# Kernel optimization log

Hardware: AMD Instinct MI355X
Metric: run time of the kernel (lower is better)

Reference implementation:

```python
import jax, jax.numpy as jnp
import numpy as np

U, I, D = 100000, 50000, 64       # users, items, latdim
H, DH = 4, 16                      # att_head, head dim (D = H*DH)
HN = 128                           # hyperNum
L = 2                              # hgnn_layer
HOPS = 2                           # gcn_hops
SLOPE = 0.5                        # leaky
NNZ_UI = 1000000
NNZ_UU = 1000000


def leaky(x):
    return jnp.where(x >= 0, x, SLOPE * x)


def spmm(rows, cols, vals, X, n_out):
    # sparse COO @ dense: out[r] += vals * X[c]
    return jax.ops.segment_sum(vals[:, None] * X[cols], rows, num_segments=n_out)


def lightgcn(uE, iE, ar, ac, av, tr, tc, tv):
    ulats, ilats = [uE], [iE]
    for _ in range(HOPS):
        tu = spmm(ar, ac, av, ilats[-1], U)
        ti = spmm(tr, tc, tv, ulats[-1], I)
        ulats.append(tu)
        ilats.append(ti)
    return sum(ulats[1:]), sum(ilats[1:])


def lightgcn2(uE, ur, uc, uv):
    lats = [uE]
    for _ in range(HOPS):
        lats.append(spmm(ur, uc, uv, lats[-1], U))
    return sum(lats[1:])


def prepare_key(E, K):
    # [N, D] -> [H, N, DH]
    return (E @ K).reshape(-1, H, DH).transpose(1, 0, 2)


def hg_transformer(E0, Key, Hyper, V, pV, W1, W2):
    # Hyper: [HN, D]; Key: [H, N, DH]
    hyp = Hyper.reshape(HN, H, DH).transpose(1, 2, 0)  # [H, DH, HN]
    total = E0
    cur = E0
    for l in range(L):
        value = (cur @ pV).reshape(-1, H, DH).transpose(1, 2, 0)   # [H, DH, N]
        t1 = ((value @ Key) @ hyp).reshape(D, HN)                  # [D, HN]
        t2 = leaky(t1 @ W1[l].T) + t1                              # Linear(HN,HN) no bias
        t3 = leaky(t2 @ W2[l].T) + t2
        pre = (t3.T @ V).reshape(HN, H, DH).transpose(1, 0, 2)     # [H, HN, DH]
        pre = hyp @ pre                                            # [H, DH, DH]
        new = (Key @ pre).transpose(1, 0, 2).reshape(-1, D)        # [N, D]
        total = total + new
        cur = new
    return total, Hyper


def setup_inputs() -> dict:
    key = jax.random.key(0)
    ks = jax.random.split(key, 14)
    s = 0.05
    uEmbeds0 = jax.random.normal(ks[0], (U, D), jnp.float32) * s
    iEmbeds0 = jax.random.normal(ks[1], (I, D), jnp.float32) * s
    Ks = jax.random.normal(ks[2], (3, D, D), jnp.float32) * (1.0 / np.sqrt(D))
    hg_Hyper = jax.random.normal(ks[3], (3, HN, D), jnp.float32) * s
    hg_V = jax.random.normal(ks[4], (3, D, D), jnp.float32) * (1.0 / np.sqrt(D))
    hg_pV = jax.random.normal(ks[5], (3, D, D), jnp.float32) * (1.0 / np.sqrt(D))
    hg_W1 = jax.random.normal(ks[6], (3, L, HN, HN), jnp.float32) * (1.0 / np.sqrt(HN))
    hg_W2 = jax.random.normal(ks[7], (3, L, HN, HN), jnp.float32) * (1.0 / np.sqrt(HN))
    adj_rows = jax.random.randint(ks[8], (NNZ_UI,), 0, U, jnp.int32)
    adj_cols = jax.random.randint(ks[9], (NNZ_UI,), 0, I, jnp.int32)
    adj_vals = jax.random.uniform(ks[10], (NNZ_UI,), jnp.float32)
    uu_rows = jax.random.randint(ks[11], (NNZ_UU,), 0, U, jnp.int32)
    uu_cols = jax.random.randint(ks[12], (NNZ_UU,), 0, U, jnp.int32)
    uu_vals = jax.random.uniform(ks[13], (NNZ_UU,), jnp.float32)
    return dict(uEmbeds0=uEmbeds0, iEmbeds0=iEmbeds0, Ks=Ks, hg_Hyper=hg_Hyper,
                hg_V=hg_V, hg_pV=hg_pV, hg_W1=hg_W1, hg_W2=hg_W2,
                adj_rows=adj_rows, adj_cols=adj_cols, adj_vals=adj_vals,
                tp_rows=adj_cols, tp_cols=adj_rows, tp_vals=adj_vals,
                uu_rows=uu_rows, uu_cols=uu_cols, uu_vals=uu_vals)


def reference(uEmbeds0, iEmbeds0, Ks, hg_Hyper, hg_V, hg_pV, hg_W1, hg_W2,
              adj_vals, tp_vals, uu_vals,
              adj_rows, adj_cols, tp_rows, tp_cols, uu_rows, uu_cols):
    ui_u_gcn, ui_i_gcn = lightgcn(uEmbeds0, iEmbeds0, adj_rows, adj_cols, adj_vals,
                                  tp_rows, tp_cols, tp_vals)
    uu_gcn = lightgcn2(uEmbeds0, uu_rows, uu_cols, uu_vals)
    ui_uEmbed0 = uEmbeds0 + ui_u_gcn
    ui_iEmbed0 = iEmbeds0 + ui_i_gcn
    uu_Embed0 = uEmbeds0 + uu_gcn
    ui_uKey = prepare_key(ui_uEmbed0, Ks[0])
    ui_iKey = prepare_key(ui_iEmbed0, Ks[1])
    uu_Key = prepare_key(uu_Embed0, Ks[2])
    ui_ulat, ui_uHyper = hg_transformer(ui_uEmbed0, ui_uKey, hg_Hyper[0], hg_V[0], hg_pV[0], hg_W1[0], hg_W2[0])
    ui_ilat, ui_iHyper = hg_transformer(ui_iEmbed0, ui_iKey, hg_Hyper[1], hg_V[1], hg_pV[1], hg_W1[1], hg_W2[1])
    uu_lat, uu_Hyper = hg_transformer(uu_Embed0, uu_Key, hg_Hyper[2], hg_V[2], hg_pV[2], hg_W1[2], hg_W2[2])
    return (ui_uEmbed0, ui_iEmbed0, ui_ulat, ui_ilat, ui_uKey, ui_iKey,
            ui_uHyper, ui_iHyper, uu_Embed0, uu_lat, uu_Key, uu_Hyper)
```

## Files before the change

kernel.cpp:

```cpp
#include <hip/hip_runtime.h>

__global__ __launch_bounds__(256) void spmm_k(const int* __restrict__ rows,
                                              const int* __restrict__ cols,
                                              const float* __restrict__ vals,
                                              const float* __restrict__ X,
                                              float* __restrict__ out, int nnz) {
    int gid = blockIdx.x * 256 + threadIdx.x;
    int e = gid >> 6;
    if (e >= nnz) return;
    int d = gid & 63;
    int r = rows[e], c = cols[e];
    float v = vals[e];
    float x = X[(size_t)c * 64 + d];
    atomicAdd(&out[(size_t)r * 64 + d], v * x);
}

__global__ __launch_bounds__(256) void add3_kernel(const float* __restrict__ base,
                                                   const float* __restrict__ a,
                                                   const float* __restrict__ b,
                                                   float* __restrict__ outb, size_t n) {
    size_t i = (size_t)blockIdx.x * 256 + threadIdx.x;
    if (i >= n) return;
    outb[i] = base[i] + a[i] + b[i];
}

__global__ __launch_bounds__(256) void hist_k(const int* __restrict__ rows,
                                              int* __restrict__ cnt, int nnz) {
    int i = blockIdx.x * 256 + threadIdx.x;
    if (i < nnz) atomicAdd(&cnt[rows[i]], 1);
}

__global__ __launch_bounds__(256) void scan_part(const int* __restrict__ cnt,
                                                 int* __restrict__ bsum, int n) {
    __shared__ int sh[256];
    int tid = threadIdx.x;
    int i = blockIdx.x * 256 + tid;
    sh[tid] = (i < n) ? cnt[i] : 0;
    __syncthreads();
    for (int st = 128; st > 0; st >>= 1) {
        if (tid < st) sh[tid] += sh[tid + st];
        __syncthreads();
    }
    if (tid == 0) bsum[blockIdx.x] = sh[0];
}

__global__ __launch_bounds__(1024) void scan_top(int* __restrict__ b, int nb) {
    __shared__ int sh[1024];
    int tid = threadIdx.x;
    int orig = (tid < nb) ? b[tid] : 0;
    sh[tid] = orig;
    __syncthreads();
    for (int st = 1; st < 1024; st <<= 1) {
        int v = (tid >= st) ? sh[tid - st] : 0;
        __syncthreads();
        sh[tid] += v;
        __syncthreads();
    }
    if (tid < nb) b[tid] = sh[tid] - orig;
}

__global__ __launch_bounds__(256) void scan_final(const int* __restrict__ cnt,
                                                  const int* __restrict__ bsum,
                                                  int* __restrict__ rp,
                                                  int* __restrict__ cur, int n, int nnz) {
    __shared__ int sh[256];
    int tid = threadIdx.x;
    int i = blockIdx.x * 256 + tid;
    int orig = (i < n) ? cnt[i] : 0;
    sh[tid] = orig;
    __syncthreads();
    for (int st = 1; st < 256; st <<= 1) {
        int v = (tid >= st) ? sh[tid - st] : 0;
        __syncthreads();
        sh[tid] += v;
        __syncthreads();
    }
    int ex = sh[tid] - orig + bsum[blockIdx.x];
    if (i < n) { rp[i] = ex; cur[i] = ex; }
    if (i == n - 1) rp[n] = nnz;
}

__global__ __launch_bounds__(256) void scatter_k(const int* __restrict__ rows,
                                                 const int* __restrict__ cols,
                                                 const float* __restrict__ vals,
                                                 int* __restrict__ cur,
                                                 int2* __restrict__ edge, int nnz) {
    int i = blockIdx.x * 256 + threadIdx.x;
    if (i >= nnz) return;
    int p = atomicAdd(&cur[rows[i]], 1);
    edge[p] = make_int2(cols[i], __float_as_int(vals[i]));
}

__global__ __launch_bounds__(256) void spmm_csr(const int* __restrict__ rp,
                                                const int2* __restrict__ edge,
                                                const float* __restrict__ X,
                                                const float* __restrict__ a0,
                                                const float* __restrict__ a1,
                                                float* __restrict__ out, int nrows) {
    int gid = blockIdx.x * 256 + threadIdx.x;
    int r = gid >> 6;
    if (r >= nrows) return;
    int d = gid & 63;
    int s = rp[r], e = rp[r + 1];
    float acc = 0.f;
    int i = s;
    for (; i + 4 <= e; i += 4) {
        int2 e0 = edge[i], e1 = edge[i + 1], e2 = edge[i + 2], e3 = edge[i + 3];
        float x0 = X[(size_t)e0.x * 64 + d];
        float x1 = X[(size_t)e1.x * 64 + d];
        float x2 = X[(size_t)e2.x * 64 + d];
        float x3 = X[(size_t)e3.x * 64 + d];
        acc += __int_as_float(e0.y) * x0;
        acc += __int_as_float(e1.y) * x1;
        acc += __int_as_float(e2.y) * x2;
        acc += __int_as_float(e3.y) * x3;
    }
    for (; i < e; ++i) {
        int2 ee = edge[i];
        acc += __int_as_float(ee.y) * X[(size_t)ee.x * 64 + d];
    }
    size_t o = (size_t)r * 64 + d;
    if (a0) acc += a0[o];
    if (a1) acc += a1[o];
    out[o] = acc;
}

__global__ __launch_bounds__(256) void key_gemm(const float* __restrict__ E,
                                                const float* __restrict__ K,
                                                float* __restrict__ Kout, int N) {
    __shared__ float Ksh[4096];
    int tid = threadIdx.x;
    for (int i = tid; i < 4096; i += 256) Ksh[i] = K[i];
    __syncthreads();
    int j = tid & 63, slot = tid >> 6;
    int n = blockIdx.x * 4 + slot;
    if (n >= N) return;
    const float* Er = E + (size_t)n * 64;
    float acc = 0.f;
#pragma unroll
    for (int kk = 0; kk < 64; ++kk) acc += Er[kk] * Ksh[kk * 64 + j];
    int h = j >> 4, dh = j & 15;
    Kout[((size_t)h * N + n) * 16 + dh] = acc;
}

#define ATB_BLOCKS 512
__global__ __launch_bounds__(256) void atb_part(const float* __restrict__ cur,
                                                const float* __restrict__ Key,
                                                float* __restrict__ part, int N, int chunk) {
    int tid = threadIdx.x;
    int k = tid & 63, h = tid >> 6;
    const float* Kh = Key + (size_t)h * N * 16;
    float acc[16];
#pragma unroll
    for (int i = 0; i < 16; ++i) acc[i] = 0.f;
    int s = blockIdx.x * chunk;
    int e = s + chunk;
    if (e > N) e = N;
#pragma unroll 2
    for (int n = s; n < e; ++n) {
        float c = cur[(size_t)n * 64 + k];
        const float4* kr = (const float4*)(Kh + (size_t)n * 16);
        float4 k0 = kr[0], k1 = kr[1], k2 = kr[2], k3 = kr[3];
        acc[0]  += c * k0.x;  acc[1]  += c * k0.y;  acc[2]  += c * k0.z;  acc[3]  += c * k0.w;
        acc[4]  += c * k1.x;  acc[5]  += c * k1.y;  acc[6]  += c * k1.z;  acc[7]  += c * k1.w;
        acc[8]  += c * k2.x;  acc[9]  += c * k2.y;  acc[10] += c * k2.z;  acc[11] += c * k2.w;
        acc[12] += c * k3.x;  acc[13] += c * k3.y;  acc[14] += c * k3.z;  acc[15] += c * k3.w;
    }
    float4* po = (float4*)(part + (size_t)blockIdx.x * 4096 + k * 64 + h * 16);
    po[0] = make_float4(acc[0],  acc[1],  acc[2],  acc[3]);
    po[1] = make_float4(acc[4],  acc[5],  acc[6],  acc[7]);
    po[2] = make_float4(acc[8],  acc[9],  acc[10], acc[11]);
    po[3] = make_float4(acc[12], acc[13], acc[14], acc[15]);
}

__global__ __launch_bounds__(256) void reduce_m(const float* __restrict__ part,
                                                float* __restrict__ M, int nb) {
    int i = blockIdx.x * 256 + threadIdx.x;
    if (i >= 4096) return;
    float s = 0.f;
#pragma unroll 8
    for (int b = 0; b < nb; ++b) s += part[(size_t)b * 4096 + i];
    M[i] = s;
}

#define ATB_ROWS 128
__global__ __launch_bounds__(256) void atb_k(const float* __restrict__ cur,
                                             const float* __restrict__ Key,
                                             float* __restrict__ M, int N) {
    int tid = threadIdx.x;
    int k = tid & 63, h = tid >> 6;
    const float* Kh = Key + (size_t)h * N * 16;
    float acc[16];
#pragma unroll
    for (int i = 0; i < 16; ++i) acc[i] = 0.f;
    int s = blockIdx.x * ATB_ROWS;
    int e = s + ATB_ROWS;
    if (e > N) e = N;
#pragma unroll 2
    for (int n = s; n < e; ++n) {
        float c = cur[(size_t)n * 64 + k];
        const float4* kr = (const float4*)(Kh + (size_t)n * 16);
        float4 k0 = kr[0], k1 = kr[1], k2 = kr[2], k3 = kr[3];
        acc[0]  += c * k0.x;  acc[1]  += c * k0.y;  acc[2]  += c * k0.z;  acc[3]  += c * k0.w;
        acc[4]  += c * k1.x;  acc[5]  += c * k1.y;  acc[6]  += c * k1.z;  acc[7]  += c * k1.w;
        acc[8]  += c * k2.x;  acc[9]  += c * k2.y;  acc[10] += c * k2.z;  acc[11] += c * k2.w;
        acc[12] += c * k3.x;  acc[13] += c * k3.y;  acc[14] += c * k3.z;  acc[15] += c * k3.w;
    }
#pragma unroll
    for (int d2 = 0; d2 < 16; ++d2)
        atomicAdd(&M[k * 64 + h * 16 + d2], acc[d2]);
}

__global__ __launch_bounds__(256) void vk_small(const float* __restrict__ M,
                                                const float* __restrict__ pV,
                                                float* __restrict__ VK) {
    int i = blockIdx.x * 256 + threadIdx.x;
    if (i >= 1024) return;
    int d2 = i & 15, d1 = (i >> 4) & 15, h = i >> 8;
    float s = 0.f;
#pragma unroll
    for (int k = 0; k < 64; ++k)
        s += pV[k * 64 + h * 16 + d1] * M[k * 64 + h * 16 + d2];
    VK[i] = s;
}

__global__ __launch_bounds__(256) void t1_kernel(const float* __restrict__ VK,
                                                 const float* __restrict__ hyp,
                                                 float* __restrict__ t1) {
    int i = blockIdx.x * 256 + threadIdx.x;
    if (i >= 8192) return;
    int m = i & 127, d = i >> 7;
    int h = d >> 4;
    float s = 0.f;
#pragma unroll
    for (int d2 = 0; d2 < 16; ++d2) s += VK[d * 16 + d2] * hyp[(h * 16 + d2) * 128 + m];
    t1[i] = s;
}

__global__ __launch_bounds__(256) void ff_kernel(const float* __restrict__ tin,
                                                 const float* __restrict__ W,
                                                 float* __restrict__ tout) {
    int i = blockIdx.x * 256 + threadIdx.x;
    if (i >= 8192) return;
    int m = i & 127, d = i >> 7;
    const float* tr = tin + d * 128;
    const float* wr = W + m * 128;
    float s = 0.f;
#pragma unroll
    for (int mm = 0; mm < 128; ++mm) s += tr[mm] * wr[mm];
    float v = (s >= 0.f ? s : 0.5f * s) + tin[i];
    tout[i] = v;
}

__global__ __launch_bounds__(256) void pre0_kernel(const float* __restrict__ t3,
                                                   const float* __restrict__ V,
                                                   float* __restrict__ pre0) {
    int i = blockIdx.x * 256 + threadIdx.x;
    if (i >= 8192) return;
    int dd = i & 63, m = i >> 6;
    float s = 0.f;
#pragma unroll
    for (int d = 0; d < 64; ++d) s += t3[d * 128 + m] * V[d * 64 + dd];
    pre0[m * 64 + dd] = s;
}

__global__ __launch_bounds__(256) void pre2_kernel(const float* __restrict__ hyp,
                                                   const float* __restrict__ pre0,
                                                   float* __restrict__ pre2) {
    int i = blockIdx.x * 256 + threadIdx.x;
    if (i >= 1024) return;
    int d2 = i & 15, d1 = (i >> 4) & 15, h = i >> 8;
    float s = 0.f;
#pragma unroll
    for (int m = 0; m < 128; ++m) s += hyp[(h * 16 + d1) * 128 + m] * pre0[m * 64 + h * 16 + d2];
    pre2[i] = s;
}

__global__ __launch_bounds__(256) void expand0_kernel(const float* __restrict__ Key,
                                                      const float* __restrict__ pre2,
                                                      const float* __restrict__ E0,
                                                      float* __restrict__ nxt,
                                                      float* __restrict__ tot, int N) {
    __shared__ float p2[1024];
    int tid = threadIdx.x;
    for (int i = tid; i < 1024; i += 256) p2[i] = pre2[i];
    __syncthreads();
    int j = tid & 63, slot = tid >> 6;
    int n = blockIdx.x * 4 + slot;
    if (n >= N) return;
    int h = j >> 4, d2 = j & 15;
    const float* kr = Key + ((size_t)h * N + n) * 16;
    float s = 0.f;
#pragma unroll
    for (int d1 = 0; d1 < 16; ++d1) s += kr[d1] * p2[(h * 16 + d1) * 16 + d2];
    size_t o = (size_t)n * 64 + j;
    nxt[o] = s;
    tot[o] = E0[o] + s;
}

__global__ __launch_bounds__(256) void expand1_kernel(const float* __restrict__ Key,
                                                      const float* __restrict__ pre2,
                                                      const float* __restrict__ tot,
                                                      float* __restrict__ outb, int N) {
    __shared__ float p2[1024];
    int tid = threadIdx.x;
    for (int i = tid; i < 1024; i += 256) p2[i] = pre2[i];
    __syncthreads();
    int j = tid & 63, slot = tid >> 6;
    int n = blockIdx.x * 4 + slot;
    if (n >= N) return;
    int h = j >> 4, d2 = j & 15;
    const float* kr = Key + ((size_t)h * N + n) * 16;
    float s = 0.f;
#pragma unroll
    for (int d1 = 0; d1 < 16; ++d1) s += kr[d1] * p2[(h * 16 + d1) * 16 + d2];
    size_t o = (size_t)n * 64 + j;
    outb[o] = tot[o] + s;
}

__global__ __launch_bounds__(256) void hyp_kernel(const float* __restrict__ Hyper,
                                                  float* __restrict__ hyp3,
                                                  float* __restrict__ out,
                                                  size_t off0, size_t off1, size_t off2) {
    int i = blockIdx.x * 256 + threadIdx.x;
    if (i >= 3 * 8192) return;
    int k = i / 8192, r = i % 8192;
    float v = Hyper[i];
    size_t off = (k == 0) ? off0 : ((k == 1) ? off1 : off2);
    out[off + r] = v;
    int m = r >> 6, dcol = r & 63;
    hyp3[k * 8192 + dcol * 128 + m] = v;
}

extern "C" void kernel_launch(void* const* d_in, const int* in_sizes, int n_in,
                              void* d_out, int out_size, void* d_ws, size_t ws_size,
                              hipStream_t stream) {
    const float* uE      = (const float*)d_in[0];
    const float* iE      = (const float*)d_in[1];
    const float* Ks      = (const float*)d_in[2];
    const float* Hyper   = (const float*)d_in[3];
    const float* Vt      = (const float*)d_in[4];
    const float* pV      = (const float*)d_in[5];
    const float* W1      = (const float*)d_in[6];
    const float* W2      = (const float*)d_in[7];
    const int* adj_rows  = (const int*)d_in[8];
    const int* adj_cols  = (const int*)d_in[9];
    const float* adj_vals= (const float*)d_in[10];
    const int* tp_rows   = (const int*)d_in[11];
    const int* tp_cols   = (const int*)d_in[12];
    const float* tp_vals = (const float*)d_in[13];
    const int* uu_rows   = (const int*)d_in[14];
    const int* uu_cols   = (const int*)d_in[15];
    const float* uu_vals = (const float*)d_in[16];

    const int U = in_sizes[0] / 64;
    const int I = in_sizes[1] / 64;
    const int nnz_ui = in_sizes[8];
    const int nnz_uu = in_sizes[14];
    const size_t UD = (size_t)U * 64, ID = (size_t)I * 64;

    float* ws = (float*)d_ws;
    float* B1 = ws;
    float* B2 = B1 + UD;
    float* B3 = B2 + ID;
    float* hyp3 = B2;
    float* VKw  = hyp3 + 3 * 8192;
    float* t1w  = VKw + 1024;
    float* t2w  = t1w + 8192;
    float* t3w  = t2w + 8192;
    float* pre0w = t3w + 8192;
    float* pre2w = pre0w + 8192;
    float* Mw   = pre2w + 1024;

    float* csrf   = B3 + UD;
    int2*  edge_a = (int2*)csrf;
    int2*  edge_t = edge_a + nnz_ui;
    int2*  edge_u = edge_t + nnz_ui;
    int*   rp_a   = (int*)(edge_u + nnz_uu);
    int*   cur_a  = rp_a + (U + 1);
    int*   rp_t   = cur_a + U;
    int*   cur_t  = rp_t + (I + 1);
    int*   rp_u   = cur_t + I;
    int*   cur_u  = rp_u + (U + 1);
    int*   bsum_a = cur_u + U;
    int*   bsum_t = bsum_a + 1024;
    int*   bsum_u = bsum_t + 1024;
    float* partw  = (float*)(bsum_u + 1024);
    size_t need_bytes = (size_t)((char*)(partw + (size_t)ATB_BLOCKS * 4096) - (char*)d_ws);
    const bool use_csr = (ws_size >= need_bytes) &&
                         ((U + 255) / 256 <= 1024) && ((I + 255) / 256 <= 1024);

    float* out = (float*)d_out;
    const size_t o_uE0 = 0;
    const size_t o_iE0 = UD;
    const size_t o_ulat = UD + ID;
    const size_t o_ilat = 2 * UD + ID;
    const size_t o_uKey = 2 * UD + 2 * ID;
    const size_t o_iKey = 3 * UD + 2 * ID;
    const size_t o_uHyp = 3 * UD + 3 * ID;
    const size_t o_iHyp = o_uHyp + 8192;
    const size_t o_uuE0 = o_iHyp + 8192;
    const size_t o_uulat = o_uuE0 + UD;
    const size_t o_uuKey = o_uulat + UD;
    const size_t o_uuHyp = o_uuKey + UD;

    const int gEU = (int)(((size_t)U * 64 + 255) / 256);
    const int gEI = (int)(((size_t)I * 64 + 255) / 256);

    if (use_csr) {
        auto build = [&](const int* rows, const int* cols, const float* vals,
                         int nnz, int n, int* rp, int* cur, int* bsum, int2* edge) {
            int nb = (n + 255) / 256;
            hipMemsetAsync(cur, 0, (size_t)n * sizeof(int), stream);
            hist_k<<<(nnz + 255) / 256, 256, 0, stream>>>(rows, cur, nnz);
            scan_part<<<nb, 256, 0, stream>>>(cur, bsum, n);
            scan_top<<<1, 1024, 0, stream>>>(bsum, nb);
            scan_final<<<nb, 256, 0, stream>>>(cur, bsum, rp, cur, n, nnz);
            scatter_k<<<(nnz + 255) / 256, 256, 0, stream>>>(rows, cols, vals, cur, edge, nnz);
        };
        build(adj_rows, adj_cols, adj_vals, nnz_ui, U, rp_a, cur_a, bsum_a, edge_a);
        build(tp_rows,  tp_cols,  tp_vals,  nnz_ui, I, rp_t, cur_t, bsum_t, edge_t);
        build(uu_rows,  uu_cols,  uu_vals,  nnz_uu, U, rp_u, cur_u, bsum_u, edge_u);

        spmm_csr<<<gEI, 256, 0, stream>>>(rp_t, edge_t, uE, nullptr, nullptr, B2, I);
        spmm_csr<<<gEU, 256, 0, stream>>>(rp_a, edge_a, iE, nullptr, nullptr, B1, U);
        spmm_csr<<<gEU, 256, 0, stream>>>(rp_a, edge_a, B2, uE, B1, out + o_uE0, U);
        spmm_csr<<<gEI, 256, 0, stream>>>(rp_t, edge_t, B1, iE, B2, out + o_iE0, I);
        spmm_csr<<<gEU, 256, 0, stream>>>(rp_u, edge_u, uE, nullptr, nullptr, B1, U);
        spmm_csr<<<gEU, 256, 0, stream>>>(rp_u, edge_u, B1, uE, B1, out + o_uuE0, U);
    } else {
        const int g_ui = (int)(((size_t)nnz_ui * 64 + 255) / 256);
        const int g_uu = (int)(((size_t)nnz_uu * 64 + 255) / 256);
        const int gU = (int)((UD + 255) / 256);
        const int gI = (int)((ID + 255) / 256);
        hipMemsetAsync(B1, 0, UD * sizeof(float), stream);
        spmm_k<<<g_ui, 256, 0, stream>>>(adj_rows, adj_cols, adj_vals, iE, B1, nnz_ui);
        hipMemsetAsync(B2, 0, ID * sizeof(float), stream);
        spmm_k<<<g_ui, 256, 0, stream>>>(tp_rows, tp_cols, tp_vals, uE, B2, nnz_ui);
        hipMemsetAsync(B3, 0, UD * sizeof(float), stream);
        spmm_k<<<g_ui, 256, 0, stream>>>(adj_rows, adj_cols, adj_vals, B2, B3, nnz_ui);
        add3_kernel<<<gU, 256, 0, stream>>>(uE, B1, B3, out + o_uE0, UD);
        hipMemsetAsync(B3, 0, ID * sizeof(float), stream);
        spmm_k<<<g_ui, 256, 0, stream>>>(tp_rows, tp_cols, tp_vals, B1, B3, nnz_ui);
        add3_kernel<<<gI, 256, 0, stream>>>(iE, B2, B3, out + o_iE0, ID);
        hipMemsetAsync(B1, 0, UD * sizeof(float), stream);
        spmm_k<<<g_uu, 256, 0, stream>>>(uu_rows, uu_cols, uu_vals, uE, B1, nnz_uu);
        hipMemsetAsync(B3, 0, UD * sizeof(float), stream);
        spmm_k<<<g_uu, 256, 0, stream>>>(uu_rows, uu_cols, uu_vals, B1, B3, nnz_uu);
        add3_kernel<<<gU, 256, 0, stream>>>(uE, B1, B3, out + o_uuE0, UD);
    }

    hyp_kernel<<<(3 * 8192 + 255) / 256, 256, 0, stream>>>(Hyper, hyp3, out, o_uHyp, o_iHyp, o_uuHyp);

    const int    Narr[3] = { U, I, U };
    const size_t oE[3]   = { o_uE0, o_iE0, o_uuE0 };
    const size_t oK[3]   = { o_uKey, o_iKey, o_uuKey };
    const size_t oL[3]   = { o_ulat, o_ilat, o_uulat };

    for (int k = 0; k < 3; ++k) {
        int N = Narr[k];
        const float* E0k = out + oE[k];
        float* Keyk = out + oK[k];
        const float* Ksk = Ks + k * 4096;
        const float* pVk = pV + k * 4096;
        const float* Vk  = Vt + k * 4096;
        const float* hypk = hyp3 + k * 8192;

        key_gemm<<<(N + 3) / 4, 256, 0, stream>>>(E0k, Ksk, Keyk, N);

        for (int l = 0; l < 2; ++l) {
            const float* W1kl = W1 + (size_t)(k * 2 + l) * 16384;
            const float* W2kl = W2 + (size_t)(k * 2 + l) * 16384;

            if (use_csr) {
                int chunk = (N + ATB_BLOCKS - 1) / ATB_BLOCKS;
                atb_part<<<ATB_BLOCKS, 256, 0, stream>>>(
                    (l == 0) ? E0k : B1, Keyk, partw, N, chunk);
                reduce_m<<<16, 256, 0, stream>>>(partw, Mw, ATB_BLOCKS);
            } else {
                hipMemsetAsync(Mw, 0, 4096 * sizeof(float), stream);
                atb_k<<<(N + ATB_ROWS - 1) / ATB_ROWS, 256, 0, stream>>>(
                    (l == 0) ? E0k : B1, Keyk, Mw, N);
            }
            vk_small<<<4, 256, 0, stream>>>(Mw, pVk, VKw);
            t1_kernel<<<32, 256, 0, stream>>>(VKw, hypk, t1w);
            ff_kernel<<<32, 256, 0, stream>>>(t1w, W1kl, t2w);
            ff_kernel<<<32, 256, 0, stream>>>(t2w, W2kl, t3w);
            pre0_kernel<<<32, 256, 0, stream>>>(t3w, Vk, pre0w);
            pre2_kernel<<<4, 256, 0, stream>>>(hypk, pre0w, pre2w);

            if (l == 0) {
                expand0_kernel<<<(N + 3) / 4, 256, 0, stream>>>(Keyk, pre2w, E0k, B1, B3, N);
            } else {
                expand1_kernel<<<(N + 3) / 4, 256, 0, stream>>>(Keyk, pre2w, B3, out + oL[k], N);
            }
        }
    }
}
```

Baseline: 1.889 ms.

## Batch the three graph branches into combined kernels and fuse the small chain

Merges the CSR build (histogram, scan, scatter), the SpMM hops, the key GEMM, the ATB partial reductions and the expand kernels for all three branches into single launches that pick a segment from the block or row index. The per-layer chain of small matmuls (vk, t1, ff, pre0, pre2) collapses into one chain3 kernel. The aim is to cut the many kernel launches and to let the three independent branches fill the GPU together instead of running one after another. The cost is extra workspace for the concurrent branch buffers, plus branch selection inside the kernels, which adds complexity.

```diff
diff --git a/kernel.cpp b/kernel.cpp
--- a/kernel.cpp
+++ b/kernel.cpp
@@ -1,50 +1,46 @@
 #include <hip/hip_runtime.h>
 
-__global__ __launch_bounds__(256) void spmm_k(const int* __restrict__ rows,
-                                              const int* __restrict__ cols,
-                                              const float* __restrict__ vals,
-                                              const float* __restrict__ X,
-                                              float* __restrict__ out, int nnz) {
-    int gid = blockIdx.x * 256 + threadIdx.x;
-    int e = gid >> 6;
-    if (e >= nnz) return;
-    int d = gid & 63;
-    int r = rows[e], c = cols[e];
-    float v = vals[e];
-    float x = X[(size_t)c * 64 + d];
-    atomicAdd(&out[(size_t)r * 64 + d], v * x);
-}
-
-__global__ __launch_bounds__(256) void add3_kernel(const float* __restrict__ base,
-                                                   const float* __restrict__ a,
-                                                   const float* __restrict__ b,
-                                                   float* __restrict__ outb, size_t n) {
-    size_t i = (size_t)blockIdx.x * 256 + threadIdx.x;
-    if (i >= n) return;
-    outb[i] = base[i] + a[i] + b[i];
-}
-
-__global__ __launch_bounds__(256) void hist_k(const int* __restrict__ rows,
-                                              int* __restrict__ cnt, int nnz) {
+#define ATB_B 256
+
+__global__ __launch_bounds__(256) void hist3(const int* __restrict__ rA,
+                                             const int* __restrict__ rT,
+                                             const int* __restrict__ rU,
+                                             int nnzA, int nnzU,
+                                             int* __restrict__ cntAll, int U, int I) {
     int i = blockIdx.x * 256 + threadIdx.x;
-    if (i < nnz) atomicAdd(&cnt[rows[i]], 1);
-}
-
-__global__ __launch_bounds__(256) void scan_part(const int* __restrict__ cnt,
-                                                 int* __restrict__ bsum, int n) {
+    int tot = 2 * nnzA + nnzU;
+    if (i >= tot) return;
+    if (i < nnzA) atomicAdd(&cntAll[rA[i]], 1);
+    else if (i < 2 * nnzA) atomicAdd(&cntAll[U + rT[i - nnzA]], 1);
+    else atomicAdd(&cntAll[U + I + rU[i - 2 * nnzA]], 1);
+}
+
+__global__ __launch_bounds__(256) void scan_part3(const int* __restrict__ cntAll,
+                                                  int* __restrict__ bsumAll,
+                                                  int U, int I, int nbA, int nbT) {
+    int b = blockIdx.x;
+    int k, lb, n, coff, bsoff;
+    if (b < nbA)            { k = 0; lb = b;             n = U; coff = 0;     bsoff = 0; }
+    else if (b < nbA + nbT) { k = 1; lb = b - nbA;       n = I; coff = U;     bsoff = 1024; }
+    else                    { k = 2; lb = b - nbA - nbT; n = U; coff = U + I; bsoff = 2048; }
+    (void)k;
     __shared__ int sh[256];
     int tid = threadIdx.x;
-    int i = blockIdx.x * 256 + tid;
-    sh[tid] = (i < n) ? cnt[i] : 0;
+    int i = lb * 256 + tid;
+    sh[tid] = (i < n) ? cntAll[coff + i] : 0;
     __syncthreads();
     for (int st = 128; st > 0; st >>= 1) {
         if (tid < st) sh[tid] += sh[tid + st];
         __syncthreads();
     }
-    if (tid == 0) bsum[blockIdx.x] = sh[0];
-}
-
-__global__ __launch_bounds__(1024) void scan_top(int* __restrict__ b, int nb) {
+    if (tid == 0) bsumAll[bsoff + lb] = sh[0];
+}
+
+__global__ __launch_bounds__(1024) void scan_top3(int* __restrict__ bsumAll,
+                                                  int nbA, int nbT, int nbU) {
+    int g = blockIdx.x;
+    int nb = (g == 0) ? nbA : (g == 1 ? nbT : nbU);
+    int* b = bsumAll + g * 1024;
     __shared__ int sh[1024];
     int tid = threadIdx.x;
     int orig = (tid < nb) ? b[tid] : 0;
@@ -59,14 +55,20 @@
     if (tid < nb) b[tid] = sh[tid] - orig;
 }
 
-__global__ __launch_bounds__(256) void scan_final(const int* __restrict__ cnt,
-                                                  const int* __restrict__ bsum,
-                                                  int* __restrict__ rp,
-                                                  int* __restrict__ cur, int n, int nnz) {
+__global__ __launch_bounds__(256) void scan_final3(int* __restrict__ curAll,
+                                                   const int* __restrict__ bsumAll,
+                                                   int* __restrict__ rpAll,
+                                                   int U, int I, int nbA, int nbT,
+                                                   int nnzA, int nnzU) {
+    int b = blockIdx.x;
+    int lb, n, coff, bsoff, rpoff, nnz;
+    if (b < nbA)            { lb = b;             n = U; coff = 0;     bsoff = 0;    rpoff = 0;                 nnz = nnzA; }
+    else if (b < nbA + nbT) { lb = b - nbA;       n = I; coff = U;     bsoff = 1024; rpoff = U + 1;             nnz = nnzA; }
+    else                    { lb = b - nbA - nbT; n = U; coff = U + I; bsoff = 2048; rpoff = (U + 1) + (I + 1); nnz = nnzU; }
     __shared__ int sh[256];
     int tid = threadIdx.x;
-    int i = blockIdx.x * 256 + tid;
-    int orig = (i < n) ? cnt[i] : 0;
+    int i = lb * 256 + tid;
+    int orig = (i < n) ? curAll[coff + i] : 0;
     sh[tid] = orig;
     __syncthreads();
     for (int st = 1; st < 256; st <<= 1) {
@@ -75,37 +77,51 @@
         sh[tid] += v;
         __syncthreads();
     }
-    int ex = sh[tid] - orig + bsum[blockIdx.x];
-    if (i < n) { rp[i] = ex; cur[i] = ex; }
-    if (i == n - 1) rp[n] = nnz;
-}
-
-__global__ __launch_bounds__(256) void scatter_k(const int* __restrict__ rows,
-                                                 const int* __restrict__ cols,
-                                                 const float* __restrict__ vals,
-                                                 int* __restrict__ cur,
-                                                 int2* __restrict__ edge, int nnz) {
+    int ex = sh[tid] - orig + bsumAll[bsoff + lb];
+    if (i < n) { rpAll[rpoff + i] = ex; curAll[coff + i] = ex; }
+    if (i == n - 1) rpAll[rpoff + n] = nnz;
+}
+
+__global__ __launch_bounds__(256) void scatter3(const int* __restrict__ rA, const int* __restrict__ cA, const float* __restrict__ vA,
+                                                const int* __restrict__ rT, const int* __restrict__ cT, const float* __restrict__ vT,
+                                                const int* __restrict__ rU, const int* __restrict__ cU, const float* __restrict__ vU,
+                                                int* __restrict__ curAll, int2* __restrict__ eAll,
+                                                int nnzA, int nnzU, int U, int I) {
     int i = blockIdx.x * 256 + threadIdx.x;
-    if (i >= nnz) return;
-    int p = atomicAdd(&cur[rows[i]], 1);
-    edge[p] = make_int2(cols[i], __float_as_int(vals[i]));
-}
-
-__global__ __launch_bounds__(256) void spmm_csr(const int* __restrict__ rp,
-                                                const int2* __restrict__ edge,
-                                                const float* __restrict__ X,
-                                                const float* __restrict__ a0,
-                                                const float* __restrict__ a1,
-                                                float* __restrict__ out, int nrows) {
+    int tot = 2 * nnzA + nnzU;
+    if (i >= tot) return;
+    if (i < nnzA) {
+        int p = atomicAdd(&curAll[rA[i]], 1);
+        eAll[p] = make_int2(cA[i], __float_as_int(vA[i]));
+    } else if (i < 2 * nnzA) {
+        int j = i - nnzA;
+        int p = atomicAdd(&curAll[U + rT[j]], 1);
+        eAll[nnzA + p] = make_int2(cT[j], __float_as_int(vT[j]));
+    } else {
+        int j = i - 2 * nnzA;
+        int p = atomicAdd(&curAll[U + I + rU[j]], 1);
+        eAll[2 * nnzA + p] = make_int2(cU[j], __float_as_int(vU[j]));
+    }
+}
+
+struct Seg { const int* rp; const int2* eg; const float* X; const float* a0; const float* a1; float* out; int N; };
+struct Spmm3Args { Seg s0, s1, s2; int n0, n01, total; };
+
+__global__ __launch_bounds__(256) void spmm3(Spmm3Args A) {
     int gid = blockIdx.x * 256 + threadIdx.x;
     int r = gid >> 6;
-    if (r >= nrows) return;
+    if (r >= A.total) return;
     int d = gid & 63;
-    int s = rp[r], e = rp[r + 1];
+    Seg sg; int lr;
+    if (r < A.n0)       { sg = A.s0; lr = r; }
+    else if (r < A.n01) { sg = A.s1; lr = r - A.n0; }
+    else                { sg = A.s2; lr = r - A.n01; }
+    int s = sg.rp[lr], e = sg.rp[lr + 1];
+    const float* __restrict__ X = sg.X;
     float acc = 0.f;
     int i = s;
     for (; i + 4 <= e; i += 4) {
-        int2 e0 = edge[i], e1 = edge[i + 1], e2 = edge[i + 2], e3 = edge[i + 3];
+        int2 e0 = sg.eg[i], e1 = sg.eg[i + 1], e2 = sg.eg[i + 2], e3 = sg.eg[i + 3];
         float x0 = X[(size_t)e0.x * 64 + d];
         float x1 = X[(size_t)e1.x * 64 + d];
         float x2 = X[(size_t)e2.x * 64 + d];
@@ -116,44 +132,56 @@
         acc += __int_as_float(e3.y) * x3;
     }
     for (; i < e; ++i) {
-        int2 ee = edge[i];
+        int2 ee = sg.eg[i];
         acc += __int_as_float(ee.y) * X[(size_t)ee.x * 64 + d];
     }
-    size_t o = (size_t)r * 64 + d;
-    if (a0) acc += a0[o];
-    if (a1) acc += a1[o];
-    out[o] = acc;
-}
-
-__global__ __launch_bounds__(256) void key_gemm(const float* __restrict__ E,
-                                                const float* __restrict__ K,
-                                                float* __restrict__ Kout, int N) {
+    size_t o = (size_t)lr * 64 + d;
+    if (sg.a0) acc += sg.a0[o];
+    if (sg.a1) acc += sg.a1[o];
+    sg.out[o] = acc;
+}
+
+struct KSeg { const float* E; const float* K; float* Kout; int N; };
+struct Key3Args { KSeg s0, s1, s2; int b1, b2; };
+
+__global__ __launch_bounds__(256) void key3(Key3Args A) {
+    int b = blockIdx.x;
+    KSeg sg; int lb;
+    if (b >= A.b2)      { sg = A.s2; lb = b - A.b2; }
+    else if (b >= A.b1) { sg = A.s1; lb = b - A.b1; }
+    else                { sg = A.s0; lb = b; }
     __shared__ float Ksh[4096];
     int tid = threadIdx.x;
-    for (int i = tid; i < 4096; i += 256) Ksh[i] = K[i];
+    for (int i = tid; i < 4096; i += 256) Ksh[i] = sg.K[i];
     __syncthreads();
     int j = tid & 63, slot = tid >> 6;
-    int n = blockIdx.x * 4 + slot;
-    if (n >= N) return;
-    const float* Er = E + (size_t)n * 64;
+    int n = lb * 4 + slot;
+    if (n >= sg.N) return;
+    const float* Er = sg.E + (size_t)n * 64;
     float acc = 0.f;
 #pragma unroll
     for (int kk = 0; kk < 64; ++kk) acc += Er[kk] * Ksh[kk * 64 + j];
     int h = j >> 4, dh = j & 15;
-    Kout[((size_t)h * N + n) * 16 + dh] = acc;
-}
-
-#define ATB_BLOCKS 512
-__global__ __launch_bounds__(256) void atb_part(const float* __restrict__ cur,
-                                                const float* __restrict__ Key,
-                                                float* __restrict__ part, int N, int chunk) {
+    sg.Kout[((size_t)h * sg.N + n) * 16 + dh] = acc;
+}
+
+__global__ __launch_bounds__(256) void atb3(const float* __restrict__ c0, const float* __restrict__ c1, const float* __restrict__ c2,
+                                            const float* __restrict__ K0, const float* __restrict__ K1, const float* __restrict__ K2,
+                                            int N0, int N1, int N2,
+                                            float* __restrict__ part) {
+    int kidx = blockIdx.x / ATB_B;
+    int lb = blockIdx.x % ATB_B;
+    const float* cur = (kidx == 0) ? c0 : (kidx == 1 ? c1 : c2);
+    const float* Key = (kidx == 0) ? K0 : (kidx == 1 ? K1 : K2);
+    int N = (kidx == 0) ? N0 : (kidx == 1 ? N1 : N2);
+    int chunk = (N + ATB_B - 1) / ATB_B;
     int tid = threadIdx.x;
     int k = tid & 63, h = tid >> 6;
     const float* Kh = Key + (size_t)h * N * 16;
     float acc[16];
 #pragma unroll
     for (int i = 0; i < 16; ++i) acc[i] = 0.f;
-    int s = blockIdx.x * chunk;
+    int s = lb * chunk;
     int e = s + chunk;
     if (e > N) e = N;
 #pragma unroll 2
@@ -166,156 +194,136 @@
         acc[8]  += c * k2.x;  acc[9]  += c * k2.y;  acc[10] += c * k2.z;  acc[11] += c * k2.w;
         acc[12] += c * k3.x;  acc[13] += c * k3.y;  acc[14] += c * k3.z;  acc[15] += c * k3.w;
     }
-    float4* po = (float4*)(part + (size_t)blockIdx.x * 4096 + k * 64 + h * 16);
+    float4* po = (float4*)(part + ((size_t)kidx * ATB_B + lb) * 4096 + k * 64 + h * 16);
     po[0] = make_float4(acc[0],  acc[1],  acc[2],  acc[3]);
     po[1] = make_float4(acc[4],  acc[5],  acc[6],  acc[7]);
     po[2] = make_float4(acc[8],  acc[9],  acc[10], acc[11]);
     po[3] = make_float4(acc[12], acc[13], acc[14], acc[15]);
 }
 
-__global__ __launch_bounds__(256) void reduce_m(const float* __restrict__ part,
-                                                float* __restrict__ M, int nb) {
-    int i = blockIdx.x * 256 + threadIdx.x;
-    if (i >= 4096) return;
+__global__ __launch_bounds__(256) void reduce3(const float* __restrict__ part,
+                                               float* __restrict__ Mall) {
+    int k = blockIdx.x >> 4;
+    int i = (blockIdx.x & 15) * 256 + threadIdx.x;
+    const float* p = part + (size_t)k * ATB_B * 4096 + i;
     float s = 0.f;
 #pragma unroll 8
-    for (int b = 0; b < nb; ++b) s += part[(size_t)b * 4096 + i];
-    M[i] = s;
-}
-
-#define ATB_ROWS 128
-__global__ __launch_bounds__(256) void atb_k(const float* __restrict__ cur,
-                                             const float* __restrict__ Key,
-                                             float* __restrict__ M, int N) {
-    int tid = threadIdx.x;
-    int k = tid & 63, h = tid >> 6;
-    const float* Kh = Key + (size_t)h * N * 16;
-    float acc[16];
-#pragma unroll
-    for (int i = 0; i < 16; ++i) acc[i] = 0.f;
-    int s = blockIdx.x * ATB_ROWS;
-    int e = s + ATB_ROWS;
-    if (e > N) e = N;
-#pragma unroll 2
-    for (int n = s; n < e; ++n) {
-        float c = cur[(size_t)n * 64 + k];
-        const float4* kr = (const float4*)(Kh + (size_t)n * 16);
-        float4 k0 = kr[0], k1 = kr[1], k2 = kr[2], k3 = kr[3];
-        acc[0]  += c * k0.x;  acc[1]  += c * k0.y;  acc[2]  += c * k0.z;  acc[3]  += c * k0.w;
-        acc[4]  += c * k1.x;  acc[5]  += c * k1.y;  acc[6]  += c * k1.z;  acc[7]  += c * k1.w;
-        acc[8]  += c * k2.x;  acc[9]  += c * k2.y;  acc[10] += c * k2.z;  acc[11] += c * k2.w;
-        acc[12] += c * k3.x;  acc[13] += c * k3.y;  acc[14] += c * k3.z;  acc[15] += c * k3.w;
-    }
-#pragma unroll
-    for (int d2 = 0; d2 < 16; ++d2)
-        atomicAdd(&M[k * 64 + h * 16 + d2], acc[d2]);
-}
-
-__global__ __launch_bounds__(256) void vk_small(const float* __restrict__ M,
-                                                const float* __restrict__ pV,
-                                                float* __restrict__ VK) {
-    int i = blockIdx.x * 256 + threadIdx.x;
-    if (i >= 1024) return;
-    int d2 = i & 15, d1 = (i >> 4) & 15, h = i >> 8;
-    float s = 0.f;
-#pragma unroll
-    for (int k = 0; k < 64; ++k)
-        s += pV[k * 64 + h * 16 + d1] * M[k * 64 + h * 16 + d2];
-    VK[i] = s;
-}
-
-__global__ __launch_bounds__(256) void t1_kernel(const float* __restrict__ VK,
-                                                 const float* __restrict__ hyp,
-                                                 float* __restrict__ t1) {
-    int i = blockIdx.x * 256 + threadIdx.x;
-    if (i >= 8192) return;
-    int m = i & 127, d = i >> 7;
-    int h = d >> 4;
-    float s = 0.f;
-#pragma unroll
-    for (int d2 = 0; d2 < 16; ++d2) s += VK[d * 16 + d2] * hyp[(h * 16 + d2) * 128 + m];
-    t1[i] = s;
-}
-
-__global__ __launch_bounds__(256) void ff_kernel(const float* __restrict__ tin,
-                                                 const float* __restrict__ W,
-                                                 float* __restrict__ tout) {
-    int i = blockIdx.x * 256 + threadIdx.x;
-    if (i >= 8192) return;
-    int m = i & 127, d = i >> 7;
-    const float* tr = tin + d * 128;
-    const float* wr = W + m * 128;
-    float s = 0.f;
-#pragma unroll
-    for (int mm = 0; mm < 128; ++mm) s += tr[mm] * wr[mm];
-    float v = (s >= 0.f ? s : 0.5f * s) + tin[i];
-    tout[i] = v;
-}
-
-__global__ __launch_bounds__(256) void pre0_kernel(const float* __restrict__ t3,
-                                                   const float* __restrict__ V,
-                                                   float* __restrict__ pre0) {
-    int i = blockIdx.x * 256 + threadIdx.x;
-    if (i >= 8192) return;
-    int dd = i & 63, m = i >> 6;
-    float s = 0.f;
-#pragma unroll
-    for (int d = 0; d < 64; ++d) s += t3[d * 128 + m] * V[d * 64 + dd];
-    pre0[m * 64 + dd] = s;
-}
-
-__global__ __launch_bounds__(256) void pre2_kernel(const float* __restrict__ hyp,
-                                                   const float* __restrict__ pre0,
-                                                   float* __restrict__ pre2) {
-    int i = blockIdx.x * 256 + threadIdx.x;
-    if (i >= 1024) return;
-    int d2 = i & 15, d1 = (i >> 4) & 15, h = i >> 8;
-    float s = 0.f;
-#pragma unroll
-    for (int m = 0; m < 128; ++m) s += hyp[(h * 16 + d1) * 128 + m] * pre0[m * 64 + h * 16 + d2];
-    pre2[i] = s;
-}
-
-__global__ __launch_bounds__(256) void expand0_kernel(const float* __restrict__ Key,
-                                                      const float* __restrict__ pre2,
-                                                      const float* __restrict__ E0,
-                                                      float* __restrict__ nxt,
-                                                      float* __restrict__ tot, int N) {
+    for (int b = 0; b < ATB_B; ++b) s += p[(size_t)b * 4096];
+    Mall[k * 4096 + i] = s;
+}
+
+__global__ __launch_bounds__(1024) void chain3(const float* __restrict__ Mall,
+                                               const float* __restrict__ pV,
+                                               const float* __restrict__ hyp3,
+                                               const float* __restrict__ W1,
+                                               const float* __restrict__ W2,
+                                               const float* __restrict__ Vt,
+                                               float* __restrict__ pre2all, int l) {
+    int kg = blockIdx.x;
+    const float* M    = Mall + kg * 4096;
+    const float* pVk  = pV + kg * 4096;
+    const float* hyp  = hyp3 + kg * 8192;
+    const float* W1kl = W1 + (size_t)(kg * 2 + l) * 16384;
+    const float* W2kl = W2 + (size_t)(kg * 2 + l) * 16384;
+    const float* Vk   = Vt + kg * 4096;
+    float* pre2 = pre2all + kg * 1024;
+
+    __shared__ float Msh[4096];
+    __shared__ float pVsh[4096];
+    __shared__ float hypsh[8192];
+    __shared__ float VKs[1024];
+    __shared__ float tA[8192];
+    __shared__ float tB[8192];
+
+    int tid = threadIdx.x;
+    for (int i = tid; i < 4096; i += 1024) { Msh[i] = M[i]; pVsh[i] = pV ? pVk[i] : 0.f; }
+    for (int i = tid; i < 8192; i += 1024) hypsh[i] = hyp[i];
+    __syncthreads();
+
+    {
+        int d2 = tid & 15, d1 = (tid >> 4) & 15, h = tid >> 8;
+        float s = 0.f;
+#pragma unroll
+        for (int k2 = 0; k2 < 64; ++k2)
+            s += pVsh[k2 * 64 + h * 16 + d1] * Msh[k2 * 64 + h * 16 + d2];
+        VKs[tid] = s;
+    }
+    __syncthreads();
+
+    for (int i = tid; i < 8192; i += 1024) {
+        int m = i & 127, d = i >> 7, h = d >> 4;
+        float s = 0.f;
+#pragma unroll
+        for (int d2 = 0; d2 < 16; ++d2) s += VKs[d * 16 + d2] * hypsh[(h * 16 + d2) * 128 + m];
+        tA[i] = s;
+    }
+    __syncthreads();
+
+    for (int i = tid; i < 8192; i += 1024) {
+        int m = i & 127, d = i >> 7;
+        const float* tr = tA + d * 128;
+        const float* wr = W1kl + m * 128;
+        float s = 0.f;
+#pragma unroll
+        for (int mm = 0; mm < 128; ++mm) s += tr[mm] * wr[mm];
+        tB[i] = (s >= 0.f ? s : 0.5f * s) + tA[i];
+    }
+    __syncthreads();
+
+    for (int i = tid; i < 8192; i += 1024) {
+        int m = i & 127, d = i >> 7;
+        const float* tr = tB + d * 128;
+        const float* wr = W2kl + m * 128;
+        float s = 0.f;
+#pragma unroll
+        for (int mm = 0; mm < 128; ++mm) s += tr[mm] * wr[mm];
+        tA[i] = (s >= 0.f ? s : 0.5f * s) + tB[i];
+    }
+    __syncthreads();
+
+    for (int i = tid; i < 8192; i += 1024) {
+        int dd = i & 63, m = i >> 6;
+        float s = 0.f;
+#pragma unroll
+        for (int d = 0; d < 64; ++d) s += tA[d * 128 + m] * Vk[d * 64 + dd];
+        tB[i] = s;
+    }
+    __syncthreads();
+
+    {
+        int d2 = tid & 15, d1 = (tid >> 4) & 15, h = tid >> 8;
+        float s = 0.f;
+#pragma unroll
+        for (int m = 0; m < 128; ++m)
+            s += hypsh[(h * 16 + d1) * 128 + m] * tB[m * 64 + h * 16 + d2];
+        pre2[tid] = s;
+    }
+}
+
+struct ESeg { const float* Key; const float* pre2; const float* in; float* out1; float* out2; int N; };
+struct Exp3Args { ESeg s0, s1, s2; int b1, b2; };
+
+__global__ __launch_bounds__(256) void expand3(Exp3Args A, int mode) {
+    int b = blockIdx.x;
+    ESeg sg; int lb;
+    if (b >= A.b2)      { sg = A.s2; lb = b - A.b2; }
+    else if (b >= A.b1) { sg = A.s1; lb = b - A.b1; }
+    else                { sg = A.s0; lb = b; }
     __shared__ float p2[1024];
     int tid = threadIdx.x;
-    for (int i = tid; i < 1024; i += 256) p2[i] = pre2[i];
+    for (int i = tid; i < 1024; i += 256) p2[i] = sg.pre2[i];
     __syncthreads();
     int j = tid & 63, slot = tid >> 6;
-    int n = blockIdx.x * 4 + slot;
-    if (n >= N) return;
+    int n = lb * 4 + slot;
+    if (n >= sg.N) return;
     int h = j >> 4, d2 = j & 15;
-    const float* kr = Key + ((size_t)h * N + n) * 16;
+    const float* kr = sg.Key + ((size_t)h * sg.N + n) * 16;
     float s = 0.f;
 #pragma unroll
     for (int d1 = 0; d1 < 16; ++d1) s += kr[d1] * p2[(h * 16 + d1) * 16 + d2];
     size_t o = (size_t)n * 64 + j;
-    nxt[o] = s;
-    tot[o] = E0[o] + s;
-}
-
-__global__ __launch_bounds__(256) void expand1_kernel(const float* __restrict__ Key,
-                                                      const float* __restrict__ pre2,
-                                                      const float* __restrict__ tot,
-                                                      float* __restrict__ outb, int N) {
-    __shared__ float p2[1024];
-    int tid = threadIdx.x;
-    for (int i = tid; i < 1024; i += 256) p2[i] = pre2[i];
-    __syncthreads();
-    int j = tid & 63, slot = tid >> 6;
-    int n = blockIdx.x * 4 + slot;
-    if (n >= N) return;
-    int h = j >> 4, d2 = j & 15;
-    const float* kr = Key + ((size_t)h * N + n) * 16;
-    float s = 0.f;
-#pragma unroll
-    for (int d1 = 0; d1 < 16; ++d1) s += kr[d1] * p2[(h * 16 + d1) * 16 + d2];
-    size_t o = (size_t)n * 64 + j;
-    outb[o] = tot[o] + s;
+    if (mode == 0) { sg.out1[o] = s; sg.out2[o] = sg.in[o] + s; }
+    else           { sg.out1[o] = sg.in[o] + s; }
 }
 
 __global__ __launch_bounds__(256) void hyp_kernel(const float* __restrict__ Hyper,
@@ -330,6 +338,179 @@
     out[off + r] = v;
     int m = r >> 6, dcol = r & 63;
     hyp3[k * 8192 + dcol * 128 + m] = v;
+}
+
+__global__ __launch_bounds__(256) void spmm_k(const int* __restrict__ rows,
+                                              const int* __restrict__ cols,
+                                              const float* __restrict__ vals,
+                                              const float* __restrict__ X,
+                                              float* __restrict__ out, int nnz) {
+    int gid = blockIdx.x * 256 + threadIdx.x;
+    int e = gid >> 6;
+    if (e >= nnz) return;
+    int d = gid & 63;
+    int r = rows[e], c = cols[e];
+    float v = vals[e];
+    atomicAdd(&out[(size_t)r * 64 + d], v * X[(size_t)c * 64 + d]);
+}
+
+__global__ __launch_bounds__(256) void add3_kernel(const float* __restrict__ base,
+                                                   const float* __restrict__ a,
+                                                   const float* __restrict__ b,
+                                                   float* __restrict__ outb, size_t n) {
+    size_t i = (size_t)blockIdx.x * 256 + threadIdx.x;
+    if (i >= n) return;
+    outb[i] = base[i] + a[i] + b[i];
+}
+
+__global__ __launch_bounds__(256) void key_gemm(const float* __restrict__ E,
+                                                const float* __restrict__ K,
+                                                float* __restrict__ Kout, int N) {
+    __shared__ float Ksh[4096];
+    int tid = threadIdx.x;
+    for (int i = tid; i < 4096; i += 256) Ksh[i] = K[i];
+    __syncthreads();
+    int j = tid & 63, slot = tid >> 6;
+    int n = blockIdx.x * 4 + slot;
+    if (n >= N) return;
+    const float* Er = E + (size_t)n * 64;
+    float acc = 0.f;
+#pragma unroll
+    for (int kk = 0; kk < 64; ++kk) acc += Er[kk] * Ksh[kk * 64 + j];
+    int h = j >> 4, dh = j & 15;
+    Kout[((size_t)h * N + n) * 16 + dh] = acc;
+}
+
+#define ATB_ROWS 128
+__global__ __launch_bounds__(256) void atb_k(const float* __restrict__ cur,
+                                             const float* __restrict__ Key,
+                                             float* __restrict__ M, int N) {
+    int tid = threadIdx.x;
+    int k = tid & 63, h = tid >> 6;
+    const float* Kh = Key + (size_t)h * N * 16;
+    float acc[16];
+#pragma unroll
+    for (int i = 0; i < 16; ++i) acc[i] = 0.f;
+    int s = blockIdx.x * ATB_ROWS;
+    int e = s + ATB_ROWS;
+    if (e > N) e = N;
+    for (int n = s; n < e; ++n) {
+        float c = cur[(size_t)n * 64 + k];
+        const float4* kr = (const float4*)(Kh + (size_t)n * 16);
+        float4 k0 = kr[0], k1 = kr[1], k2 = kr[2], k3 = kr[3];
+        acc[0]  += c * k0.x;  acc[1]  += c * k0.y;  acc[2]  += c * k0.z;  acc[3]  += c * k0.w;
+        acc[4]  += c * k1.x;  acc[5]  += c * k1.y;  acc[6]  += c * k1.z;  acc[7]  += c * k1.w;
+        acc[8]  += c * k2.x;  acc[9]  += c * k2.y;  acc[10] += c * k2.z;  acc[11] += c * k2.w;
+        acc[12] += c * k3.x;  acc[13] += c * k3.y;  acc[14] += c * k3.z;  acc[15] += c * k3.w;
+    }
+#pragma unroll
+    for (int d2 = 0; d2 < 16; ++d2)
+        atomicAdd(&M[k * 64 + h * 16 + d2], acc[d2]);
+}
+
+__global__ __launch_bounds__(256) void vk_small(const float* __restrict__ M,
+                                                const float* __restrict__ pV,
+                                                float* __restrict__ VK) {
+    int i = blockIdx.x * 256 + threadIdx.x;
+    if (i >= 1024) return;
+    int d2 = i & 15, d1 = (i >> 4) & 15, h = i >> 8;
+    float s = 0.f;
+#pragma unroll
+    for (int k = 0; k < 64; ++k)
+        s += pV[k * 64 + h * 16 + d1] * M[k * 64 + h * 16 + d2];
+    VK[i] = s;
+}
+
+__global__ __launch_bounds__(256) void t1_kernel(const float* __restrict__ VK,
+                                                 const float* __restrict__ hyp,
+                                                 float* __restrict__ t1) {
+    int i = blockIdx.x * 256 + threadIdx.x;
+    if (i >= 8192) return;
+    int m = i & 127, d = i >> 7, h = d >> 4;
+    float s = 0.f;
+#pragma unroll
+    for (int d2 = 0; d2 < 16; ++d2) s += VK[d * 16 + d2] * hyp[(h * 16 + d2) * 128 + m];
+    t1[i] = s;
+}
+
+__global__ __launch_bounds__(256) void ff_kernel(const float* __restrict__ tin,
+                                                 const float* __restrict__ W,
+                                                 float* __restrict__ tout) {
+    int i = blockIdx.x * 256 + threadIdx.x;
+    if (i >= 8192) return;
+    int m = i & 127, d = i >> 7;
+    const float* tr = tin + d * 128;
+    const float* wr = W + m * 128;
+    float s = 0.f;
+#pragma unroll
+    for (int mm = 0; mm < 128; ++mm) s += tr[mm] * wr[mm];
+    tout[i] = (s >= 0.f ? s : 0.5f * s) + tin[i];
+}
+
+__global__ __launch_bounds__(256) void pre0_kernel(const float* __restrict__ t3,
+                                                   const float* __restrict__ V,
+                                                   float* __restrict__ pre0) {
+    int i = blockIdx.x * 256 + threadIdx.x;
+    if (i >= 8192) return;
+    int dd = i & 63, m = i >> 6;
+    float s = 0.f;
+#pragma unroll
+    for (int d = 0; d < 64; ++d) s += t3[d * 128 + m] * V[d * 64 + dd];
+    pre0[m * 64 + dd] = s;
+}
+
+__global__ __launch_bounds__(256) void pre2_kernel(const float* __restrict__ hyp,
+                                                   const float* __restrict__ pre0,
+                                                   float* __restrict__ pre2) {
+    int i = blockIdx.x * 256 + threadIdx.x;
+    if (i >= 1024) return;
+    int d2 = i & 15, d1 = (i >> 4) & 15, h = i >> 8;
+    float s = 0.f;
+#pragma unroll
+    for (int m = 0; m < 128; ++m) s += hyp[(h * 16 + d1) * 128 + m] * pre0[m * 64 + h * 16 + d2];
+    pre2[i] = s;
+}
+
+__global__ __launch_bounds__(256) void expand0_kernel(const float* __restrict__ Key,
+                                                      const float* __restrict__ pre2,
+                                                      const float* __restrict__ E0,
+                                                      float* __restrict__ nxt,
+                                                      float* __restrict__ tot, int N) {
+    __shared__ float p2[1024];
+    int tid = threadIdx.x;
+    for (int i = tid; i < 1024; i += 256) p2[i] = pre2[i];
+    __syncthreads();
+    int j = tid & 63, slot = tid >> 6;
+    int n = blockIdx.x * 4 + slot;
+    if (n >= N) return;
+    int h = j >> 4, d2 = j & 15;
+    const float* kr = Key + ((size_t)h * N + n) * 16;
+    float s = 0.f;
+#pragma unroll
+    for (int d1 = 0; d1 < 16; ++d1) s += kr[d1] * p2[(h * 16 + d1) * 16 + d2];
+    size_t o = (size_t)n * 64 + j;
+    nxt[o] = s;
+    tot[o] = E0[o] + s;
+}
+
+__global__ __launch_bounds__(256) void expand1_kernel(const float* __restrict__ Key,
+                                                      const float* __restrict__ pre2,
+                                                      const float* __restrict__ tot,
+                                                      float* __restrict__ outb, int N) {
+    __shared__ float p2[1024];
+    int tid = threadIdx.x;
+    for (int i = tid; i < 1024; i += 256) p2[i] = pre2[i];
+    __syncthreads();
+    int j = tid & 63, slot = tid >> 6;
+    int n = blockIdx.x * 4 + slot;
+    if (n >= N) return;
+    int h = j >> 4, d2 = j & 15;
+    const float* kr = Key + ((size_t)h * N + n) * 16;
+    float s = 0.f;
+#pragma unroll
+    for (int d1 = 0; d1 < 16; ++d1) s += kr[d1] * p2[(h * 16 + d1) * 16 + d2];
+    size_t o = (size_t)n * 64 + j;
+    outb[o] = tot[o] + s;
 }
 
 extern "C" void kernel_launch(void* const* d_in, const int* in_sizes, int n_in,
@@ -359,37 +540,6 @@
     const int nnz_uu = in_sizes[14];
     const size_t UD = (size_t)U * 64, ID = (size_t)I * 64;
 
-    float* ws = (float*)d_ws;
-    float* B1 = ws;
-    float* B2 = B1 + UD;
-    float* B3 = B2 + ID;
-    float* hyp3 = B2;
-    float* VKw  = hyp3 + 3 * 8192;
-    float* t1w  = VKw + 1024;
-    float* t2w  = t1w + 8192;
-    float* t3w  = t2w + 8192;
-    float* pre0w = t3w + 8192;
-    float* pre2w = pre0w + 8192;
-    float* Mw   = pre2w + 1024;
-
-    float* csrf   = B3 + UD;
-    int2*  edge_a = (int2*)csrf;
-    int2*  edge_t = edge_a + nnz_ui;
-    int2*  edge_u = edge_t + nnz_ui;
-    int*   rp_a   = (int*)(edge_u + nnz_uu);
-    int*   cur_a  = rp_a + (U + 1);
-    int*   rp_t   = cur_a + U;
-    int*   cur_t  = rp_t + (I + 1);
-    int*   rp_u   = cur_t + I;
-    int*   cur_u  = rp_u + (U + 1);
-    int*   bsum_a = cur_u + U;
-    int*   bsum_t = bsum_a + 1024;
-    int*   bsum_u = bsum_t + 1024;
-    float* partw  = (float*)(bsum_u + 1024);
-    size_t need_bytes = (size_t)((char*)(partw + (size_t)ATB_BLOCKS * 4096) - (char*)d_ws);
-    const bool use_csr = (ws_size >= need_bytes) &&
-                         ((U + 255) / 256 <= 1024) && ((I + 255) / 256 <= 1024);
-
     float* out = (float*)d_out;
     const size_t o_uE0 = 0;
     const size_t o_iE0 = UD;
@@ -404,95 +554,180 @@
     const size_t o_uuKey = o_uulat + UD;
     const size_t o_uuHyp = o_uuKey + UD;
 
-    const int gEU = (int)(((size_t)U * 64 + 255) / 256);
-    const int gEI = (int)(((size_t)I * 64 + 255) / 256);
-
-    if (use_csr) {
-        auto build = [&](const int* rows, const int* cols, const float* vals,
-                         int nnz, int n, int* rp, int* cur, int* bsum, int2* edge) {
-            int nb = (n + 255) / 256;
-            hipMemsetAsync(cur, 0, (size_t)n * sizeof(int), stream);
-            hist_k<<<(nnz + 255) / 256, 256, 0, stream>>>(rows, cur, nnz);
-            scan_part<<<nb, 256, 0, stream>>>(cur, bsum, n);
-            scan_top<<<1, 1024, 0, stream>>>(bsum, nb);
-            scan_final<<<nb, 256, 0, stream>>>(cur, bsum, rp, cur, n, nnz);
-            scatter_k<<<(nnz + 255) / 256, 256, 0, stream>>>(rows, cols, vals, cur, edge, nnz);
-        };
-        build(adj_rows, adj_cols, adj_vals, nnz_ui, U, rp_a, cur_a, bsum_a, edge_a);
-        build(tp_rows,  tp_cols,  tp_vals,  nnz_ui, I, rp_t, cur_t, bsum_t, edge_t);
-        build(uu_rows,  uu_cols,  uu_vals,  nnz_uu, U, rp_u, cur_u, bsum_u, edge_u);
-
-        spmm_csr<<<gEI, 256, 0, stream>>>(rp_t, edge_t, uE, nullptr, nullptr, B2, I);
-        spmm_csr<<<gEU, 256, 0, stream>>>(rp_a, edge_a, iE, nullptr, nullptr, B1, U);
-        spmm_csr<<<gEU, 256, 0, stream>>>(rp_a, edge_a, B2, uE, B1, out + o_uE0, U);
-        spmm_csr<<<gEI, 256, 0, stream>>>(rp_t, edge_t, B1, iE, B2, out + o_iE0, I);
-        spmm_csr<<<gEU, 256, 0, stream>>>(rp_u, edge_u, uE, nullptr, nullptr, B1, U);
-        spmm_csr<<<gEU, 256, 0, stream>>>(rp_u, edge_u, B1, uE, B1, out + o_uuE0, U);
+    float* ws   = (float*)d_ws;
+    float* B1   = ws;
+    float* B2   = B1 + UD;
+    float* B3   = B2 + ID;
+    float* Ti   = B3 + UD;
+    float* Buu1 = Ti + ID;
+    float* Tuu  = Buu1 + UD;
+    float* hyp3 = Tuu + UD;
+    float* Mall = hyp3 + 24576;
+    float* pre2all = Mall + 12288;
+    int2*  edge_a = (int2*)(pre2all + 3072);
+    int2*  edge_t = edge_a + nnz_ui;
+    int2*  edge_u = edge_t + nnz_ui;
+    int*   rpAll  = (int*)(edge_u + nnz_uu);
+    int*   curAll = rpAll + (U + 1) + (I + 1) + (U + 1);
+    int*   bsumAll= curAll + U + I + U;
+    float* partw  = (float*)(bsumAll + 3072);
+    size_t need_bytes = (size_t)((char*)(partw + (size_t)3 * ATB_B * 4096) - (char*)d_ws);
+    const int nbA = (U + 255) / 256, nbT = (I + 255) / 256, nbU = (U + 255) / 256;
+    const bool use_new = (ws_size >= need_bytes) && (nbA <= 1024) && (nbT <= 1024);
+
+    int* rp_a = rpAll;
+    int* rp_t = rpAll + (U + 1);
+    int* rp_u = rpAll + (U + 1) + (I + 1);
+
+    if (use_new) {
+        hipMemsetAsync(curAll, 0, (size_t)(U + I + U) * sizeof(int), stream);
+        int totE = 2 * nnz_ui + nnz_uu;
+        hist3<<<(totE + 255) / 256, 256, 0, stream>>>(adj_rows, tp_rows, uu_rows,
+                                                      nnz_ui, nnz_uu, curAll, U, I);
+        scan_part3<<<nbA + nbT + nbU, 256, 0, stream>>>(curAll, bsumAll, U, I, nbA, nbT);
+        scan_top3<<<3, 1024, 0, stream>>>(bsumAll, nbA, nbT, nbU);
+        scan_final3<<<nbA + nbT + nbU, 256, 0, stream>>>(curAll, bsumAll, rpAll,
+                                                         U, I, nbA, nbT, nnz_ui, nnz_uu);
+        scatter3<<<(totE + 255) / 256, 256, 0, stream>>>(
+            adj_rows, adj_cols, adj_vals, tp_rows, tp_cols, tp_vals,
+            uu_rows, uu_cols, uu_vals, curAll, edge_a, nnz_ui, nnz_uu, U, I);
+
+        {
+            Spmm3Args A;
+            A.s0 = { rp_t, edge_t, uE, nullptr, nullptr, B2, I };
+            A.s1 = { rp_a, edge_a, iE, nullptr, nullptr, B1, U };
+            A.s2 = { nullptr, nullptr, nullptr, nullptr, nullptr, nullptr, 0 };
+            A.n0 = I; A.n01 = I + U; A.total = I + U;
+            spmm3<<<(int)(((size_t)A.total * 64 + 255) / 256), 256, 0, stream>>>(A);
+        }
+        {
+            Spmm3Args A;
+            A.s0 = { rp_a, edge_a, B2, uE, B1, out + o_uE0, U };
+            A.s1 = { rp_t, edge_t, B1, iE, B2, out + o_iE0, I };
+            A.s2 = { rp_u, edge_u, uE, nullptr, nullptr, Buu1, U };
+            A.n0 = U; A.n01 = U + I; A.total = U + I + U;
+            spmm3<<<(int)(((size_t)A.total * 64 + 255) / 256), 256, 0, stream>>>(A);
+        }
+        {
+            Spmm3Args A;
+            A.s0 = { rp_u, edge_u, Buu1, uE, Buu1, out + o_uuE0, U };
+            A.s1 = { nullptr, nullptr, nullptr, nullptr, nullptr, nullptr, 0 };
+            A.s2 = A.s1;
+            A.n0 = U; A.n01 = U; A.total = U;
+            spmm3<<<(int)(((size_t)A.total * 64 + 255) / 256), 256, 0, stream>>>(A);
+        }
+
+        hyp_kernel<<<(3 * 8192 + 255) / 256, 256, 0, stream>>>(Hyper, hyp3, out,
+                                                               o_uHyp, o_iHyp, o_uuHyp);
+
+        const int gb0 = (U + 3) / 4, gb1 = (I + 3) / 4, gb2 = (U + 3) / 4;
+        {
+            Key3Args A;
+            A.s0 = { out + o_uE0,  Ks,        out + o_uKey,  U };
+            A.s1 = { out + o_iE0,  Ks + 4096, out + o_iKey,  I };
+            A.s2 = { out + o_uuE0, Ks + 8192, out + o_uuKey, U };
+            A.b1 = gb0; A.b2 = gb0 + gb1;
+            key3<<<gb0 + gb1 + gb2, 256, 0, stream>>>(A);
+        }
+
+        const float* Key0 = out + o_uKey;
+        const float* Key1 = out + o_iKey;
+        const float* Key2 = out + o_uuKey;
+
+        for (int l = 0; l < 2; ++l) {
+            const float* c0 = (l == 0) ? (out + o_uE0)  : B1;
+            const float* c1 = (l == 0) ? (out + o_iE0)  : B2;
+            const float* c2 = (l == 0) ? (out + o_uuE0) : Buu1;
+
+            atb3<<<3 * ATB_B, 256, 0, stream>>>(c0, c1, c2, Key0, Key1, Key2, U, I, U, partw);
+            reduce3<<<48, 256, 0, stream>>>(partw, Mall);
+            chain3<<<3, 1024, 0, stream>>>(Mall, pV, hyp3, W1, W2, Vt, pre2all, l);
+
+            Exp3Args E;
+            E.b1 = gb0; E.b2 = gb0 + gb1;
+            if (l == 0) {
+                E.s0 = { Key0, pre2all,        out + o_uE0,  B1,   B3,  U };
+                E.s1 = { Key1, pre2all + 1024, out + o_iE0,  B2,   Ti,  I };
+                E.s2 = { Key2, pre2all + 2048, out + o_uuE0, Buu1, Tuu, U };
+                expand3<<<gb0 + gb1 + gb2, 256, 0, stream>>>(E, 0);
+            } else {
+                E.s0 = { Key0, pre2all,        B3,  out + o_ulat,  nullptr, U };
+                E.s1 = { Key1, pre2all + 1024, Ti,  out + o_ilat,  nullptr, I };
+                E.s2 = { Key2, pre2all + 2048, Tuu, out + o_uulat, nullptr, U };
+                expand3<<<gb0 + gb1 + gb2, 256, 0, stream>>>(E, 1);
+            }
+        }
     } else {
+        float* fB1 = ws;
+        float* fB2 = fB1 + UD;
+        float* fB3 = fB2 + ID;
+        float* fhyp3 = fB2;
+        float* fVK  = fhyp3 + 3 * 8192;
+        float* ft1  = fVK + 1024;
+        float* ft2  = ft1 + 8192;
+        float* ft3  = ft2 + 8192;
+        float* fpre0 = ft3 + 8192;
+        float* fpre2 = fpre0 + 8192;
+        float* fM   = fpre2 + 1024;
+
         const int g_ui = (int)(((size_t)nnz_ui * 64 + 255) / 256);
         const int g_uu = (int)(((size_t)nnz_uu * 64 + 255) / 256);
         const int gU = (int)((UD + 255) / 256);
         const int gI = (int)((ID + 255) / 256);
-        hipMemsetAsync(B1, 0, UD * sizeof(float), stream);
-        spmm_k<<<g_ui, 256, 0, stream>>>(adj_rows, adj_cols, adj_vals, iE, B1, nnz_ui);
-        hipMemsetAsync(B2, 0, ID * sizeof(float), stream);
-        spmm_k<<<g_ui, 256, 0, stream>>>(tp_rows, tp_cols, tp_vals, uE, B2, nnz_ui);
-        hipMemsetAsync(B3, 0, UD * sizeof(float), stream);
-        spmm_k<<<g_ui, 256, 0, stream>>>(adj_rows, adj_cols, adj_vals, B2, B3, nnz_ui);
-        add3_kernel<<<gU, 256, 0, stream>>>(uE, B1, B3, out + o_uE0, UD);
-        hipMemsetAsync(B3, 0, ID * sizeof(float), stream);
-        spmm_k<<<g_ui, 256, 0, stream>>>(tp_rows, tp_cols, tp_vals, B1, B3, nnz_ui);
-        add3_kernel<<<gI, 256, 0, stream>>>(iE, B2, B3, out + o_iE0, ID);
-        hipMemsetAsync(B1, 0, UD * sizeof(float), stream);
-        spmm_k<<<g_uu, 256, 0, stream>>>(uu_rows, uu_cols, uu_vals, uE, B1, nnz_uu);
-        hipMemsetAsync(B3, 0, UD * sizeof(float), stream);
-        spmm_k<<<g_uu, 256, 0, stream>>>(uu_rows, uu_cols, uu_vals, B1, B3, nnz_uu);
-        add3_kernel<<<gU, 256, 0, stream>>>(uE, B1, B3, out + o_uuE0, UD);
-    }
-
-    hyp_kernel<<<(3 * 8192 + 255) / 256, 256, 0, stream>>>(Hyper, hyp3, out, o_uHyp, o_iHyp, o_uuHyp);
-
-    const int    Narr[3] = { U, I, U };
-    const size_t oE[3]   = { o_uE0, o_iE0, o_uuE0 };
-    const size_t oK[3]   = { o_uKey, o_iKey, o_uuKey };
-    const size_t oL[3]   = { o_ulat, o_ilat, o_uulat };
-
-    for (int k = 0; k < 3; ++k) {
-        int N = Narr[k];
-        const float* E0k = out + oE[k];
-        float* Keyk = out + oK[k];
-        const float* Ksk = Ks + k * 4096;
-        const float* pVk = pV + k * 4096;
-        const float* Vk  = Vt + k * 4096;
-        const float* hypk = hyp3 + k * 8192;
-
-        key_gemm<<<(N + 3) / 4, 256, 0, stream>>>(E0k, Ksk, Keyk, N);
-
-        for (int l = 0; l < 2; ++l) {
-            const float* W1kl = W1 + (size_t)(k * 2 + l) * 16384;
-            const float* W2kl = W2 + (size_t)(k * 2 + l) * 16384;
-
-            if (use_csr) {
-                int chunk = (N + ATB_BLOCKS - 1) / ATB_BLOCKS;
-                atb_part<<<ATB_BLOCKS, 256, 0, stream>>>(
-                    (l == 0) ? E0k : B1, Keyk, partw, N, chunk);
-                reduce_m<<<16, 256, 0, stream>>>(partw, Mw, ATB_BLOCKS);
-            } else {
-                hipMemsetAsync(Mw, 0, 4096 * sizeof(float), stream);
+        hipMemsetAsync(fB1, 0, UD * sizeof(float), stream);
+        spmm_k<<<g_ui, 256, 0, stream>>>(adj_rows, adj_cols, adj_vals, iE, fB1, nnz_ui);
+        hipMemsetAsync(fB2, 0, ID * sizeof(float), stream);
+        spmm_k<<<g_ui, 256, 0, stream>>>(tp_rows, tp_cols, tp_vals, uE, fB2, nnz_ui);
+        hipMemsetAsync(fB3, 0, UD * sizeof(float), stream);
+        spmm_k<<<g_ui, 256, 0, stream>>>(adj_rows, adj_cols, adj_vals, fB2, fB3, nnz_ui);
+        add3_kernel<<<gU, 256, 0, stream>>>(uE, fB1, fB3, out + o_uE0, UD);
+        hipMemsetAsync(fB3, 0, ID * sizeof(float), stream);
+        spmm_k<<<g_ui, 256, 0, stream>>>(tp_rows, tp_cols, tp_vals, fB1, fB3, nnz_ui);
+        add3_kernel<<<gI, 256, 0, stream>>>(iE, fB2, fB3, out + o_iE0, ID);
+        hipMemsetAsync(fB1, 0, UD * sizeof(float), stream);
+        spmm_k<<<g_uu, 256, 0, stream>>>(uu_rows, uu_cols, uu_vals, uE, fB1, nnz_uu);
+        hipMemsetAsync(fB3, 0, UD * sizeof(float), stream);
+        spmm_k<<<g_uu, 256, 0, stream>>>(uu_rows, uu_cols, uu_vals, fB1, fB3, nnz_uu);
+        add3_kernel<<<gU, 256, 0, stream>>>(uE, fB1, fB3, out + o_uuE0, UD);
+
+        hyp_kernel<<<(3 * 8192 + 255) / 256, 256, 0, stream>>>(Hyper, fhyp3, out,
+                                                               o_uHyp, o_iHyp, o_uuHyp);
+
+        const int    Narr[3] = { U, I, U };
+        const size_t oE[3]   = { o_uE0, o_iE0, o_uuE0 };
+        const size_t oK[3]   = { o_uKey, o_iKey, o_uuKey };
+        const size_t oL[3]   = { o_ulat, o_ilat, o_uulat };
+
+        for (int k = 0; k < 3; ++k) {
+            int N = Narr[k];
+            const float* E0k = out + oE[k];
+            float* Keyk = out + oK[k];
+            const float* Ksk = Ks + k * 4096;
+            const float* pVk = pV + k * 4096;
+            const float* Vk  = Vt + k * 4096;
+            const float* hypk = fhyp3 + k * 8192;
+
+            key_gemm<<<(N + 3) / 4, 256, 0, stream>>>(E0k, Ksk, Keyk, N);
+
+            for (int l = 0; l < 2; ++l) {
+                const float* W1kl = W1 + (size_t)(k * 2 + l) * 16384;
+                const float* W2kl = W2 + (size_t)(k * 2 + l) * 16384;
+
+                hipMemsetAsync(fM, 0, 4096 * sizeof(float), stream);
                 atb_k<<<(N + ATB_ROWS - 1) / ATB_ROWS, 256, 0, stream>>>(
-                    (l == 0) ? E0k : B1, Keyk, Mw, N);
-            }
-            vk_small<<<4, 256, 0, stream>>>(Mw, pVk, VKw);
-            t1_kernel<<<32, 256, 0, stream>>>(VKw, hypk, t1w);
-            ff_kernel<<<32, 256, 0, stream>>>(t1w, W1kl, t2w);
-            ff_kernel<<<32, 256, 0, stream>>>(t2w, W2kl, t3w);
-            pre0_kernel<<<32, 256, 0, stream>>>(t3w, Vk, pre0w);
-            pre2_kernel<<<4, 256, 0, stream>>>(hypk, pre0w, pre2w);
-
-            if (l == 0) {
-                expand0_kernel<<<(N + 3) / 4, 256, 0, stream>>>(Keyk, pre2w, E0k, B1, B3, N);
-            } else {
-                expand1_kernel<<<(N + 3) / 4, 256, 0, stream>>>(Keyk, pre2w, B3, out + oL[k], N);
+                    (l == 0) ? E0k : fB1, Keyk, fM, N);
+                vk_small<<<4, 256, 0, stream>>>(fM, pVk, fVK);
+                t1_kernel<<<32, 256, 0, stream>>>(fVK, hypk, ft1);
+                ff_kernel<<<32, 256, 0, stream>>>(ft1, W1kl, ft2);
+                ff_kernel<<<32, 256, 0, stream>>>(ft2, W2kl, ft3);
+                pre0_kernel<<<32, 256, 0, stream>>>(ft3, Vk, fpre0);
+                pre2_kernel<<<4, 256, 0, stream>>>(hypk, fpre0, fpre2);
+
+                if (l == 0) {
+                    expand0_kernel<<<(N + 3) / 4, 256, 0, stream>>>(Keyk, fpre2, E0k, fB1, fB3, N);
+                } else {
+                    expand1_kernel<<<(N + 3) / 4, 256, 0, stream>>>(Keyk, fpre2, fB3, out + oL[k], N);
+                }
             }
         }
     }
```

Result: slower. 2.050 ms (+8.5%).
